# Optimization experiments

Hardware: AMD Instinct MI355X
Metric: run time of the kernel (lower is better)

## Reference

```python
import jax, jax.numpy as jnp
import numpy as np

D_MODEL = 768
N_HEADS = 12
D_K = 768
D_V = 768
SEQ = 2048
BATCH = 2


def setup_inputs() -> dict:
    key = jax.random.key(0)
    ks = jax.random.split(key, 9)
    s = 0.02
    return {
        "x": jax.random.normal(ks[0], (SEQ, BATCH, D_MODEL), dtype=jnp.float32),
        "Wq": jax.random.normal(ks[1], (D_MODEL, D_K), dtype=jnp.float32) * s,
        "bq": jnp.zeros((D_K,), dtype=jnp.float32),
        "Wk": jax.random.normal(ks[2], (D_MODEL, D_K), dtype=jnp.float32) * s,
        "bk": jnp.zeros((D_K,), dtype=jnp.float32),
        "Wv": jax.random.normal(ks[3], (D_MODEL, D_V), dtype=jnp.float32) * s,
        "bv": jnp.zeros((D_V,), dtype=jnp.float32),
        "Wo": jax.random.normal(ks[4], (D_V, D_MODEL), dtype=jnp.float32) * s,
        "bo": jnp.zeros((D_MODEL,), dtype=jnp.float32),
    }


def reference(x, Wq, bq, Wk, bk, Wv, bv, Wo, bo):
    # x: (S, B, D)
    S, B, D = x.shape
    H = N_HEADS
    hk = D_K // H
    hv = D_V // H
    q = (x @ Wq + bq).reshape(S, B, H, hk)
    k = (x @ Wk + bk).reshape(S, B, H, hk)
    v = (x @ Wv + bv).reshape(S, B, H, hv)
    scale = 1.0 / np.sqrt(hk).astype(np.float32)
    # scores: (B, H, S_q, S_k)
    att = jnp.einsum("sbhd,tbhd->bhst", q, k) * scale
    causal = jnp.triu(jnp.ones((S, S), dtype=bool), k=1)  # True above diagonal
    att = jnp.where(causal, jnp.float32(-jnp.inf), att)
    att = jax.nn.softmax(att, axis=-1)
    y = jnp.einsum("bhst,tbhd->sbhd", att, v).reshape(S, B, D_V)
    return y @ Wo + bo  # (S, B, D)
```

## Files before the change

kernel.cpp:

```cpp
#include <hip/hip_runtime.h>

typedef __attribute__((ext_vector_type(8))) short short8;
typedef __attribute__((ext_vector_type(4))) float f32x4;

#define NHEADS 12
#define SEQLEN 2048
#define HEADD  64
#define DMODEL 768

__device__ __forceinline__ short cvtbf(float f) {
  unsigned u = __builtin_bit_cast(unsigned, f);
  u += 0x7fffu + ((u >> 16) & 1u);
  return (short)(u >> 16);
}

__device__ __forceinline__ void gload16(const void* g, void* l) {
  __builtin_amdgcn_global_load_lds((const __attribute__((address_space(1))) void*)g,
                                   (__attribute__((address_space(3))) void*)l, 16, 0, 0);
}

__global__ void cvt_x_kernel(const float* __restrict__ x, short* __restrict__ o) {
  int i = blockIdx.x * 256 + threadIdx.x;
  const float* p = x + (size_t)i * 8;
  short8 v;
#pragma unroll
  for (int j = 0; j < 8; ++j) v[j] = cvtbf(p[j]);
  *(short8*)(o + (size_t)i * 8) = v;
}

__global__ void transpose_w_kernel(const float* __restrict__ w0, const float* __restrict__ w1,
                                   const float* __restrict__ w2, const float* __restrict__ w3,
                                   short* __restrict__ wt, short* __restrict__ wot) {
  __shared__ float t[32][33];
  const float* W = blockIdx.z == 0 ? w0 : blockIdx.z == 1 ? w1 : blockIdx.z == 2 ? w2 : w3;
  short* O = blockIdx.z < 3 ? wt + (size_t)blockIdx.z * (768 * 768) : wot;
  int tx = threadIdx.x, ty = threadIdx.y;
  int n0 = blockIdx.x * 32, k0 = blockIdx.y * 32;
#pragma unroll
  for (int j = 0; j < 4; ++j)
    t[ty + j * 8][tx] = W[(k0 + ty + j * 8) * 768 + n0 + tx];
  __syncthreads();
#pragma unroll
  for (int j = 0; j < 4; ++j)
    O[(n0 + ty + j * 8) * 768 + k0 + tx] = cvtbf(t[tx][ty + j * 8]);
}

template <int BN>
__device__ __forceinline__ void gemm_core64(const short* __restrict__ A,
                                            const short* __restrict__ Bt,
                                            short* sA, short* sB,
                                            int bm, int bn, f32x4 acc[2][BN / 32]) {
  constexpr int NT = BN / 32;
  const int tid = threadIdx.x;
  const int w = tid >> 6, lane = tid & 63;
  const int quad = lane >> 4, l16 = lane & 15;
  const int wm = (w & 1) * 32, wn = (w >> 1) * (BN / 2);

  int gA[2], lA[2], gB[NT], lB[NT];
#pragma unroll
  for (int j = 0; j < 2; ++j) {
    int slot = j * 256 + w * 64 + lane;
    int r = slot >> 3, c = (slot & 7) ^ (r & 7);
    gA[j] = (bm * 64 + r) * 768 + c * 8;
    lA[j] = (j * 256 + w * 64) * 8;
  }
#pragma unroll
  for (int j = 0; j < NT; ++j) {
    int slot = j * 256 + w * 64 + lane;
    int r = slot >> 3, c = (slot & 7) ^ (r & 7);
    gB[j] = (bn * BN + r) * 768 + c * 8;
    lB[j] = (j * 256 + w * 64) * 8;
  }

  for (int kt = 0; kt < 12; ++kt) {
    __syncthreads();
#pragma unroll
    for (int j = 0; j < 2; ++j) gload16(A + gA[j] + kt * 64, sA + lA[j]);
#pragma unroll
    for (int j = 0; j < NT; ++j) gload16(Bt + gB[j] + kt * 64, sB + lB[j]);
    __syncthreads();
#pragma unroll
    for (int ks = 0; ks < 2; ++ks) {
      short8 a[2], b[NT];
      int cp = (ks * 4 + quad) ^ (l16 & 7);
#pragma unroll
      for (int mt = 0; mt < 2; ++mt)
        a[mt] = *(const short8*)(sA + (wm + mt * 16 + l16) * 64 + cp * 8);
#pragma unroll
      for (int nt = 0; nt < NT; ++nt)
        b[nt] = *(const short8*)(sB + (wn + nt * 16 + l16) * 64 + cp * 8);
#pragma unroll
      for (int mt = 0; mt < 2; ++mt)
#pragma unroll
        for (int nt = 0; nt < NT; ++nt)
          acc[mt][nt] = __builtin_amdgcn_mfma_f32_16x16x32_bf16(a[mt], b[nt], acc[mt][nt], 0, 0, 0);
    }
  }
}

__global__ __launch_bounds__(256, 4) void qkv_gemm(
    const short* __restrict__ A, const short* __restrict__ Bt,
    const float* __restrict__ bq, const float* __restrict__ bk, const float* __restrict__ bv,
    short* __restrict__ oq, short* __restrict__ ok, short* __restrict__ ov) {
  __shared__ short sA[64 * 64];
  __shared__ short sB[128 * 64];
  f32x4 acc[2][4];
  const f32x4 z4 = {0.f, 0.f, 0.f, 0.f};
#pragma unroll
  for (int mt = 0; mt < 2; ++mt)
#pragma unroll
    for (int nt = 0; nt < 4; ++nt) acc[mt][nt] = z4;

  const int bm = blockIdx.x, bn = blockIdx.y;
  gemm_core64<128>(A, Bt, sA, sB, bm, bn, acc);

  const int seg = bn / 6, bn_l = bn % 6;
  const float* bias = seg == 0 ? bq : seg == 1 ? bk : bv;
  short* outp = seg == 0 ? oq : seg == 1 ? ok : ov;

  const int tid = threadIdx.x;
  const int w = tid >> 6, lane = tid & 63;
  const int quad = lane >> 4, l16 = lane & 15;
  const int wm = (w & 1) * 32, wn = (w >> 1) * 64;

#pragma unroll
  for (int nt = 0; nt < 4; ++nt) {
    int n = bn_l * 128 + wn + nt * 16 + l16;
    float bval = bias[n];
    int h = n >> 6, d = n & 63;
#pragma unroll
    for (int mt = 0; mt < 2; ++mt) {
      int rowb = wm + mt * 16 + quad * 4;
#pragma unroll
      for (int r = 0; r < 4; ++r) {
        int m = bm * 64 + rowb + r;
        int s = m >> 1, b = m & 1;
        float v = acc[mt][nt][r] + bval;
        if (seg < 2)
          outp[((b * NHEADS + h) * SEQLEN + s) * HEADD + d] = cvtbf(v);
        else
          outp[((b * NHEADS + h) * HEADD + d) * SEQLEN + s] = cvtbf(v);
      }
    }
  }
}

#define AE(qi, ts, nt) ((qi) | ((ts) << 8) | ((nt) << 16))
__device__ const int ATTN_TAB[48] = {
  AE(15,0,16), AE(16,0,16), AE(17,0,16), AE(18,0,16), AE(19,0,16), AE(20,0,16),
  AE(21,0,16), AE(22,0,16), AE(23,0,16), AE(24,0,16), AE(25,0,16), AE(26,0,16),
  AE(27,0,16), AE(28,0,16), AE(29,0,16), AE(30,0,16), AE(31,0,16), AE(31,16,16),
  AE(14,0,15), AE(30,16,15),
  AE(13,0,14), AE(29,16,14),
  AE(12,0,13), AE(28,16,13),
  AE(11,0,12), AE(27,16,12),
  AE(10,0,11), AE(26,16,11),
  AE( 9,0,10), AE(25,16,10),
  AE( 8,0, 9), AE(24,16, 9),
  AE( 7,0, 8), AE(23,16, 8),
  AE( 6,0, 7), AE(22,16, 7),
  AE( 5,0, 6), AE(21,16, 6),
  AE( 4,0, 5), AE(20,16, 5),
  AE( 3,0, 4), AE(19,16, 4),
  AE( 2,0, 3), AE(18,16, 3),
  AE( 1,0, 2), AE(17,16, 2),
  AE( 0,0, 1), AE(16,16, 1),
};

__global__ __launch_bounds__(256, 6) void attn_kernel(
    const short* __restrict__ Q, const short* __restrict__ K,
    const short* __restrict__ Vt, short* __restrict__ Y,
    float* __restrict__ Of, float* __restrict__ lf) {
  __shared__ short sK[64 * 64];
  __shared__ short sV[64 * 64];
  __shared__ short sP[64 * 64];
  const int tid = threadIdx.x;
  const int w = tid >> 6, lane = tid & 63;
  const int quad = lane >> 4, l16 = lane & 15;
  const int e = ATTN_TAB[blockIdx.x / 24];
  const int bh = blockIdx.x % 24;
  const int qi = e & 255, ts = (e >> 8) & 255, ntl = e >> 16;
  const int q0 = qi << 6;
  const short* Qb = Q + (size_t)bh * (SEQLEN * HEADD);
  const short* Kb = K + (size_t)bh * (SEQLEN * HEADD);
  const short* Vb = Vt + (size_t)bh * (SEQLEN * HEADD);

  short8 aq[2];
#pragma unroll
  for (int ks = 0; ks < 2; ++ks)
    aq[ks] = *(const short8*)(Qb + (q0 + w * 16 + l16) * 64 + ks * 32 + quad * 8);

  float l_lane[4] = {0.f, 0.f, 0.f, 0.f};
  f32x4 acc_o[4];
  const f32x4 z4 = {0.f, 0.f, 0.f, 0.f};
#pragma unroll
  for (int nt = 0; nt < 4; ++nt) acc_o[nt] = z4;

  int gK[2], gV[2], lbase[2];
#pragma unroll
  for (int j = 0; j < 2; ++j) {
    int slot = j * 256 + w * 64 + lane;
    int r = slot >> 3, c = (slot & 7) ^ (r & 7);
    gK[j] = r * 64 + c * 8;
    gV[j] = r * 2048 + c * 8;
    lbase[j] = (j * 256 + w * 64) * 8;
  }

  const int qrow = q0 + w * 16 + quad * 4;
  const float SC = 0.125f * 1.44269504089f;

  for (int it = ts; it < ts + ntl; ++it) {
    const int t0 = it << 6;
    __syncthreads();
#pragma unroll
    for (int j = 0; j < 2; ++j) {
      gload16(Kb + t0 * 64 + gK[j], sK + lbase[j]);
      gload16(Vb + t0 + gV[j], sV + lbase[j]);
    }
    __syncthreads();

    f32x4 sc[4];
#pragma unroll
    for (int nt = 0; nt < 4; ++nt) sc[nt] = z4;
#pragma unroll
    for (int ks = 0; ks < 2; ++ks) {
      int cp = (ks * 4 + quad) ^ (l16 & 7);
#pragma unroll
      for (int nt = 0; nt < 4; ++nt) {
        short8 bk = *(const short8*)(sK + (nt * 16 + l16) * 64 + cp * 8);
        sc[nt] = __builtin_amdgcn_mfma_f32_16x16x32_bf16(aq[ks], bk, sc[nt], 0, 0, 0);
      }
    }

    if (it == qi) {
#pragma unroll
      for (int nt = 0; nt < 4; ++nt)
#pragma unroll
        for (int r = 0; r < 4; ++r) {
          int t = t0 + nt * 16 + l16;
          if (t > qrow + r) sc[nt][r] = -1e30f;
        }
    }

#pragma unroll
    for (int nt = 0; nt < 4; ++nt)
#pragma unroll
      for (int r = 0; r < 4; ++r) {
        float p = __builtin_amdgcn_exp2f(sc[nt][r] * SC);
        l_lane[r] += p;
        int rq = w * 16 + quad * 4 + r;
        int t = nt * 16 + l16;
        int c = t >> 3;
        sP[rq * 64 + ((c ^ (rq & 7)) * 8 + (t & 7))] = cvtbf(p);
      }

#pragma unroll
    for (int kst = 0; kst < 2; ++kst) {
      int rq = w * 16 + l16;
      int cpa = (kst * 4 + quad) ^ (rq & 7);
      short8 ap = *(const short8*)(sP + rq * 64 + cpa * 8);
#pragma unroll
      for (int nt = 0; nt < 4; ++nt) {
        int row = nt * 16 + l16;
        int cv = (kst * 4 + quad) ^ (row & 7);
        short8 bv = *(const short8*)(sV + row * 64 + cv * 8);
        acc_o[nt] = __builtin_amdgcn_mfma_f32_16x16x32_bf16(ap, bv, acc_o[nt], 0, 0, 0);
      }
    }
  }

#pragma unroll
  for (int off = 1; off <= 8; off <<= 1)
#pragma unroll
    for (int r = 0; r < 4; ++r) l_lane[r] += __shfl_xor(l_lane[r], off);

  if (qi < 16) {
    const int b = bh / NHEADS, h = bh % NHEADS;
#pragma unroll
    for (int r = 0; r < 4; ++r) {
      float rl = __builtin_amdgcn_rcpf(l_lane[r]);
      int srow = q0 + w * 16 + quad * 4 + r;
#pragma unroll
      for (int nt = 0; nt < 4; ++nt)
        Y[(srow * 2 + b) * DMODEL + h * 64 + nt * 16 + l16] = cvtbf(acc_o[nt][r] * rl);
    }
  } else {
    const int c = (ts == 0) ? 0 : 1;
    const int slot = (bh * 16 + (qi - 16)) * 2 + c;
    float* Ob = Of + (size_t)slot * 4096;
#pragma unroll
    for (int r = 0; r < 4; ++r) {
      int row = w * 16 + quad * 4 + r;
#pragma unroll
      for (int nt = 0; nt < 4; ++nt)
        Ob[row * 64 + nt * 16 + l16] = acc_o[nt][r];
      if (l16 == 0) lf[slot * 64 + row] = l_lane[r];
    }
  }
}

__global__ void attn_merge(const float* __restrict__ Of, const float* __restrict__ lf,
                           short* __restrict__ Y) {
  const int bh = blockIdx.x % 24, qi = 16 + blockIdx.x / 24;
  const int slot = (bh * 16 + (qi - 16)) * 2;
  const float* O0 = Of + (size_t)slot * 4096;
  const float* O1 = O0 + 4096;
  const float* L0 = lf + slot * 64;
  const int b = bh / NHEADS, h = bh % NHEADS;
  const int tid = threadIdx.x;
#pragma unroll
  for (int j = 0; j < 16; ++j) {
    int idx = j * 256 + tid;
    int row = idx >> 6, col = idx & 63;
    float l = L0[row] + L0[64 + row];
    float v = (O0[idx] + O1[idx]) * __builtin_amdgcn_rcpf(l);
    int srow = qi * 64 + row;
    Y[(srow * 2 + b) * DMODEL + h * 64 + col] = cvtbf(v);
  }
}

__global__ __launch_bounds__(256, 4) void oproj_gemm(
    const short* __restrict__ A, const short* __restrict__ Bt,
    const float* __restrict__ bo, float* __restrict__ out) {
  __shared__ short sA[64 * 64];
  __shared__ short sB[64 * 64];
  f32x4 acc[2][2];
  const f32x4 z4 = {0.f, 0.f, 0.f, 0.f};
#pragma unroll
  for (int mt = 0; mt < 2; ++mt)
#pragma unroll
    for (int nt = 0; nt < 2; ++nt) acc[mt][nt] = z4;

  const int bm = blockIdx.x, bn = blockIdx.y;
  gemm_core64<64>(A, Bt, sA, sB, bm, bn, acc);

  const int tid = threadIdx.x;
  const int w = tid >> 6, lane = tid & 63;
  const int quad = lane >> 4, l16 = lane & 15;
  const int wm = (w & 1) * 32, wn = (w >> 1) * 32;

#pragma unroll
  for (int nt = 0; nt < 2; ++nt) {
    int n = bn * 64 + wn + nt * 16 + l16;
    float bval = bo[n];
#pragma unroll
    for (int mt = 0; mt < 2; ++mt) {
      int rowb = wm + mt * 16 + quad * 4;
#pragma unroll
      for (int r = 0; r < 4; ++r) {
        int m = bm * 64 + rowb + r;
        out[(size_t)m * 768 + n] = acc[mt][nt][r] + bval;
      }
    }
  }
}

extern "C" void kernel_launch(void* const* d_in, const int* in_sizes, int n_in,
                              void* d_out, int out_size, void* d_ws, size_t ws_size,
                              hipStream_t stream) {
  const float* x  = (const float*)d_in[0];
  const float* Wq = (const float*)d_in[1];
  const float* bq = (const float*)d_in[2];
  const float* Wk = (const float*)d_in[3];
  const float* bk = (const float*)d_in[4];
  const float* Wv = (const float*)d_in[5];
  const float* bv = (const float*)d_in[6];
  const float* Wo = (const float*)d_in[7];
  const float* bo = (const float*)d_in[8];
  float* out = (float*)d_out;

  short* ws  = (short*)d_ws;
  short* xb  = ws;
  short* wt  = ws + 3145728;
  short* wot = ws + 4915200;
  short* qw  = ws + 5505024;
  short* kw  = ws + 8650752;
  short* vw  = ws + 11796480;
  short* yw  = ws + 14942208;
  float* Of  = (float*)(ws + 18087936);
  float* lf  = Of + 3145728;

  cvt_x_kernel<<<1536, 256, 0, stream>>>(x, xb);
  transpose_w_kernel<<<dim3(24, 24, 4), dim3(32, 8), 0, stream>>>(Wq, Wk, Wv, Wo, wt, wot);
  qkv_gemm<<<dim3(64, 18), 256, 0, stream>>>(xb, wt, bq, bk, bv, qw, kw, vw);
  attn_kernel<<<1152, 256, 0, stream>>>(qw, kw, vw, yw, Of, lf);
  attn_merge<<<384, 256, 0, stream>>>(Of, lf, yw);
  oproj_gemm<<<dim3(64, 12), 256, 0, stream>>>(yw, wot, bo, out);
}
```

Measured before the change: 170.0 us.

## Split attention into 8-tile chunks, double-buffer K/V, fold scale into Q

Attention work is repartitioned into chunks of at most 8 KV tiles (1920 blocks), and the merge kernel sums a variable number of partials. K/V tiles are double-buffered so the next tile's loads overlap compute, with one barrier per iteration. The softmax scale and log2e are folded into Q at projection time, the row sum is computed by an MFMA against a ones vector, and P is written with a high-half store that truncates instead of rounding. The aim is better load balance and less latency and VALU work, at the cost of more partial-output traffic, lower occupancy and truncated bf16 for P.

```diff
diff --git a/kernel.cpp b/kernel.cpp
--- a/kernel.cpp
+++ b/kernel.cpp
@@ -17,6 +17,11 @@
 __device__ __forceinline__ void gload16(const void* g, void* l) {
   __builtin_amdgcn_global_load_lds((const __attribute__((address_space(1))) void*)g,
                                    (__attribute__((address_space(3))) void*)l, 16, 0, 0);
+}
+
+__device__ __forceinline__ void ds_write_hi16(short* p, float v) {
+  asm volatile("ds_write_b16_d16_hi %0, %1"
+               : : "v"((__attribute__((address_space(3))) short*)p), "v"(v) : "memory");
 }
 
 __global__ void cvt_x_kernel(const float* __restrict__ x, short* __restrict__ o) {
@@ -136,6 +141,7 @@
         int m = bm * 64 + rowb + r;
         int s = m >> 1, b = m & 1;
         float v = acc[mt][nt][r] + bval;
+        if (seg == 0) v *= 0.1803368801f;
         if (seg < 2)
           outp[((b * NHEADS + h) * SEQLEN + s) * HEADD + d] = cvtbf(v);
         else
@@ -146,33 +152,46 @@
 }
 
 #define AE(qi, ts, nt) ((qi) | ((ts) << 8) | ((nt) << 16))
-__device__ const int ATTN_TAB[48] = {
-  AE(15,0,16), AE(16,0,16), AE(17,0,16), AE(18,0,16), AE(19,0,16), AE(20,0,16),
-  AE(21,0,16), AE(22,0,16), AE(23,0,16), AE(24,0,16), AE(25,0,16), AE(26,0,16),
-  AE(27,0,16), AE(28,0,16), AE(29,0,16), AE(30,0,16), AE(31,0,16), AE(31,16,16),
-  AE(14,0,15), AE(30,16,15),
-  AE(13,0,14), AE(29,16,14),
-  AE(12,0,13), AE(28,16,13),
-  AE(11,0,12), AE(27,16,12),
-  AE(10,0,11), AE(26,16,11),
-  AE( 9,0,10), AE(25,16,10),
-  AE( 8,0, 9), AE(24,16, 9),
-  AE( 7,0, 8), AE(23,16, 8),
-  AE( 6,0, 7), AE(22,16, 7),
-  AE( 5,0, 6), AE(21,16, 6),
-  AE( 4,0, 5), AE(20,16, 5),
-  AE( 3,0, 4), AE(19,16, 4),
-  AE( 2,0, 3), AE(18,16, 3),
-  AE( 1,0, 2), AE(17,16, 2),
-  AE( 0,0, 1), AE(16,16, 1),
+__device__ const int ATTN_TAB[80] = {
+  AE(31,0,8), AE(31,8,8), AE(31,16,8), AE(31,24,8),
+  AE(30,0,8), AE(30,8,8), AE(30,16,8),
+  AE(29,0,8), AE(29,8,8), AE(29,16,8),
+  AE(28,0,8), AE(28,8,8), AE(28,16,8),
+  AE(27,0,8), AE(27,8,8), AE(27,16,8),
+  AE(26,0,8), AE(26,8,8), AE(26,16,8),
+  AE(25,0,8), AE(25,8,8), AE(25,16,8),
+  AE(24,0,8), AE(24,8,8), AE(24,16,8),
+  AE(23,0,8), AE(23,8,8), AE(23,16,8),
+  AE(22,0,8), AE(22,8,8),
+  AE(21,0,8), AE(21,8,8),
+  AE(20,0,8), AE(20,8,8),
+  AE(19,0,8), AE(19,8,8),
+  AE(18,0,8), AE(18,8,8),
+  AE(17,0,8), AE(17,8,8),
+  AE(16,0,8), AE(16,8,8),
+  AE(15,0,8), AE(15,8,8),
+  AE(14,0,8), AE(13,0,8), AE(12,0,8), AE(11,0,8),
+  AE(10,0,8), AE(9,0,8),  AE(8,0,8),  AE(7,0,8),
+  AE(30,24,7), AE(22,16,7), AE(14,8,7), AE(6,0,7),
+  AE(29,24,6), AE(21,16,6), AE(13,8,6), AE(5,0,6),
+  AE(28,24,5), AE(20,16,5), AE(12,8,5), AE(4,0,5),
+  AE(27,24,4), AE(19,16,4), AE(11,8,4), AE(3,0,4),
+  AE(26,24,3), AE(18,16,3), AE(10,8,3), AE(2,0,3),
+  AE(25,24,2), AE(17,16,2), AE(9,8,2),  AE(1,0,2),
+  AE(24,24,1), AE(16,16,1), AE(8,8,1),  AE(0,0,1),
 };
-
-__global__ __launch_bounds__(256, 6) void attn_kernel(
+__device__ const int PBASE[32] = {
+  0,0,0,0,0,0,0,0,
+  0,2,4,6,8,10,12,14,
+  16,19,22,25,28,31,34,37,
+  40,44,48,52,56,60,64,68};
+
+__global__ __launch_bounds__(256, 4) void attn_kernel(
     const short* __restrict__ Q, const short* __restrict__ K,
     const short* __restrict__ Vt, short* __restrict__ Y,
     float* __restrict__ Of, float* __restrict__ lf) {
-  __shared__ short sK[64 * 64];
-  __shared__ short sV[64 * 64];
+  __shared__ short sK[2][64 * 64];
+  __shared__ short sV[2][64 * 64];
   __shared__ short sP[64 * 64];
   const int tid = threadIdx.x;
   const int w = tid >> 6, lane = tid & 63;
@@ -190,11 +209,12 @@
   for (int ks = 0; ks < 2; ++ks)
     aq[ks] = *(const short8*)(Qb + (q0 + w * 16 + l16) * 64 + ks * 32 + quad * 8);
 
-  float l_lane[4] = {0.f, 0.f, 0.f, 0.f};
-  f32x4 acc_o[4];
+  const short8 bones = {0x3F80, 0x3F80, 0x3F80, 0x3F80, 0x3F80, 0x3F80, 0x3F80, 0x3F80};
+  f32x4 acc_o[4], acc_l;
   const f32x4 z4 = {0.f, 0.f, 0.f, 0.f};
 #pragma unroll
   for (int nt = 0; nt < 4; ++nt) acc_o[nt] = z4;
+  acc_l = z4;
 
   int gK[2], gV[2], lbase[2];
 #pragma unroll
@@ -207,17 +227,27 @@
   }
 
   const int qrow = q0 + w * 16 + quad * 4;
-  const float SC = 0.125f * 1.44269504089f;
-
-  for (int it = ts; it < ts + ntl; ++it) {
-    const int t0 = it << 6;
+  const int tend = ts + ntl;
+
+#pragma unroll
+  for (int j = 0; j < 2; ++j) {
+    gload16(Kb + (ts << 6) * 64 + gK[j], &sK[0][lbase[j]]);
+    gload16(Vb + (ts << 6) + gV[j], &sV[0][lbase[j]]);
+  }
+
+  int pb = 0;
+  for (int it = ts; it < tend; ++it) {
     __syncthreads();
-#pragma unroll
-    for (int j = 0; j < 2; ++j) {
-      gload16(Kb + t0 * 64 + gK[j], sK + lbase[j]);
-      gload16(Vb + t0 + gV[j], sV + lbase[j]);
-    }
-    __syncthreads();
+    if (it + 1 < tend) {
+      const int t1 = (it + 1) << 6;
+#pragma unroll
+      for (int j = 0; j < 2; ++j) {
+        gload16(Kb + t1 * 64 + gK[j], &sK[pb ^ 1][lbase[j]]);
+        gload16(Vb + t1 + gV[j], &sV[pb ^ 1][lbase[j]]);
+      }
+    }
+    const short* sk = sK[pb];
+    const short* sv = sV[pb];
 
     f32x4 sc[4];
 #pragma unroll
@@ -227,12 +257,13 @@
       int cp = (ks * 4 + quad) ^ (l16 & 7);
 #pragma unroll
       for (int nt = 0; nt < 4; ++nt) {
-        short8 bk = *(const short8*)(sK + (nt * 16 + l16) * 64 + cp * 8);
+        short8 bk = *(const short8*)(sk + (nt * 16 + l16) * 64 + cp * 8);
         sc[nt] = __builtin_amdgcn_mfma_f32_16x16x32_bf16(aq[ks], bk, sc[nt], 0, 0, 0);
       }
     }
 
     if (it == qi) {
+      const int t0 = it << 6;
 #pragma unroll
       for (int nt = 0; nt < 4; ++nt)
 #pragma unroll
@@ -246,12 +277,11 @@
     for (int nt = 0; nt < 4; ++nt)
 #pragma unroll
       for (int r = 0; r < 4; ++r) {
-        float p = __builtin_amdgcn_exp2f(sc[nt][r] * SC);
-        l_lane[r] += p;
+        float p = __builtin_amdgcn_exp2f(sc[nt][r]);
         int rq = w * 16 + quad * 4 + r;
         int t = nt * 16 + l16;
         int c = t >> 3;
-        sP[rq * 64 + ((c ^ (rq & 7)) * 8 + (t & 7))] = cvtbf(p);
+        ds_write_hi16(&sP[rq * 64 + ((c ^ (rq & 7)) * 8 + (t & 7))], p);
       }
 
 #pragma unroll
@@ -259,34 +289,30 @@
       int rq = w * 16 + l16;
       int cpa = (kst * 4 + quad) ^ (rq & 7);
       short8 ap = *(const short8*)(sP + rq * 64 + cpa * 8);
+      acc_l = __builtin_amdgcn_mfma_f32_16x16x32_bf16(ap, bones, acc_l, 0, 0, 0);
 #pragma unroll
       for (int nt = 0; nt < 4; ++nt) {
         int row = nt * 16 + l16;
         int cv = (kst * 4 + quad) ^ (row & 7);
-        short8 bv = *(const short8*)(sV + row * 64 + cv * 8);
+        short8 bv = *(const short8*)(sv + row * 64 + cv * 8);
         acc_o[nt] = __builtin_amdgcn_mfma_f32_16x16x32_bf16(ap, bv, acc_o[nt], 0, 0, 0);
       }
     }
-  }
-
-#pragma unroll
-  for (int off = 1; off <= 8; off <<= 1)
-#pragma unroll
-    for (int r = 0; r < 4; ++r) l_lane[r] += __shfl_xor(l_lane[r], off);
-
-  if (qi < 16) {
+    pb ^= 1;
+  }
+
+  if (qi < 8) {
     const int b = bh / NHEADS, h = bh % NHEADS;
 #pragma unroll
     for (int r = 0; r < 4; ++r) {
-      float rl = __builtin_amdgcn_rcpf(l_lane[r]);
+      float rl = __builtin_amdgcn_rcpf(acc_l[r]);
       int srow = q0 + w * 16 + quad * 4 + r;
 #pragma unroll
       for (int nt = 0; nt < 4; ++nt)
         Y[(srow * 2 + b) * DMODEL + h * 64 + nt * 16 + l16] = cvtbf(acc_o[nt][r] * rl);
     }
   } else {
-    const int c = (ts == 0) ? 0 : 1;
-    const int slot = (bh * 16 + (qi - 16)) * 2 + c;
+    const int slot = bh * 72 + PBASE[qi] + (ts >> 3);
     float* Ob = Of + (size_t)slot * 4096;
 #pragma unroll
     for (int r = 0; r < 4; ++r) {
@@ -294,26 +320,30 @@
 #pragma unroll
       for (int nt = 0; nt < 4; ++nt)
         Ob[row * 64 + nt * 16 + l16] = acc_o[nt][r];
-      if (l16 == 0) lf[slot * 64 + row] = l_lane[r];
+      if (l16 == 0) lf[slot * 64 + row] = acc_l[r];
     }
   }
 }
 
 __global__ void attn_merge(const float* __restrict__ Of, const float* __restrict__ lf,
                            short* __restrict__ Y) {
-  const int bh = blockIdx.x % 24, qi = 16 + blockIdx.x / 24;
-  const int slot = (bh * 16 + (qi - 16)) * 2;
-  const float* O0 = Of + (size_t)slot * 4096;
-  const float* O1 = O0 + 4096;
-  const float* L0 = lf + slot * 64;
+  const int bh = blockIdx.x % 24, qi = 8 + blockIdx.x / 24;
+  const int nch = (qi >> 3) + 1;
+  const int base = bh * 72 + PBASE[qi];
+  const float* O0 = Of + (size_t)base * 4096;
+  const float* L0 = lf + base * 64;
   const int b = bh / NHEADS, h = bh % NHEADS;
   const int tid = threadIdx.x;
 #pragma unroll
   for (int j = 0; j < 16; ++j) {
     int idx = j * 256 + tid;
     int row = idx >> 6, col = idx & 63;
-    float l = L0[row] + L0[64 + row];
-    float v = (O0[idx] + O1[idx]) * __builtin_amdgcn_rcpf(l);
+    float o = 0.f, l = 0.f;
+    for (int c = 0; c < nch; ++c) {
+      o += O0[c * 4096 + idx];
+      l += L0[c * 64 + row];
+    }
+    float v = o * __builtin_amdgcn_rcpf(l);
     int srow = qi * 64 + row;
     Y[(srow * 2 + b) * DMODEL + h * 64 + col] = cvtbf(v);
   }
@@ -378,12 +408,12 @@
   short* vw  = ws + 11796480;
   short* yw  = ws + 14942208;
   float* Of  = (float*)(ws + 18087936);
-  float* lf  = Of + 3145728;
+  float* lf  = Of + 7077888;
 
   cvt_x_kernel<<<1536, 256, 0, stream>>>(x, xb);
   transpose_w_kernel<<<dim3(24, 24, 4), dim3(32, 8), 0, stream>>>(Wq, Wk, Wv, Wo, wt, wot);
   qkv_gemm<<<dim3(64, 18), 256, 0, stream>>>(xb, wt, bq, bk, bv, qw, kw, vw);
-  attn_kernel<<<1152, 256, 0, stream>>>(qw, kw, vw, yw, Of, lf);
-  attn_merge<<<384, 256, 0, stream>>>(Of, lf, yw);
+  attn_kernel<<<1920, 256, 0, stream>>>(qw, kw, vw, yw, Of, lf);
+  attn_merge<<<576, 256, 0, stream>>>(Of, lf, yw);
   oproj_gemm<<<dim3(64, 12), 256, 0, stream>>>(yw, wot, bo, out);
 }
```

Measured after the change: 167.7 us. Within noise of the previous version (-1.3%).
